# Performance work log

Measured on AMD Instinct MI355X. Metric: run time of the kernel, lower is better.

Reference implementation:

```python
import math
import jax, jax.numpy as jnp
import numpy as np

NUM_HEADS = 12


def _key_blocks(x, w):
    # x: [B,S,H,D] -> overlapping key blocks [B, C, 3w, H, D], block c covers
    # original key positions [c*w - w, c*w + 2w) (zero padded at the edges).
    B, S, H, D = x.shape
    C = S // w
    x_pad = jnp.pad(x, ((0, 0), (w, w), (0, 0), (0, 0)))
    idx = (jnp.arange(C) * w)[:, None] + jnp.arange(3 * w)[None, :]  # [C,3w]
    return x_pad[:, idx]


def _band_qk(q, k, w):
    # banded_gemm_qk: scores[b,i,h,j] = q[b,i,h,:] . k[b,i+j-w,h,:], j in [0,2w]
    B, S, H, D = q.shape
    C = S // w
    kb = _key_blocks(k, w)                       # [B,C,3w,H,D]
    qb = q.reshape(B, C, w, H, D)
    s = jnp.einsum('bcxhd,bcyhd->bchxy', qb, kb)  # [B,C,H,w,3w]
    row = jnp.arange(w)[:, None]
    col = row + jnp.arange(2 * w + 1)[None, :]    # diagonal extraction
    band = s[:, :, :, row, col]                   # [B,C,H,w,2w+1]
    return band.transpose(0, 1, 3, 2, 4).reshape(B, S, H, 2 * w + 1)


def _band_pv(p, v, w):
    # banded_gemm_pv: out[b,i,h,:] = sum_j p[b,i,h,j] * v[b,i+j-w,h,:]
    B, S, H, M = p.shape
    C = S // w
    vb = _key_blocks(v, w)                        # [B,C,3w,H,D]
    pb = p.reshape(B, C, w, H, M).transpose(0, 1, 3, 2, 4)  # [B,C,H,w,2w+1]
    row = jnp.arange(w)[:, None]
    col = row + jnp.arange(2 * w + 1)[None, :]
    p_full = jnp.zeros((B, C, H, w, 3 * w), p.dtype).at[:, :, :, row, col].set(pb)
    out = jnp.einsum('bchxy,bcyhd->bcxhd', p_full, vb)  # [B,C,w,H,D]
    return out.reshape(B, S, H, -1)


def setup_inputs():
    key = jax.random.key(0)
    ks = jax.random.split(key, 14)
    B, S, E, G = 2, 4096, 768, 64
    scale = 0.02
    hs = jax.random.normal(ks[0], (B, S, E), jnp.float32)
    mask = jnp.zeros((B, 1, 1, S), jnp.int32).at[:, :, :, :G].set(1)
    def lin(k):
        kw, kb = jax.random.split(k)
        return (jax.random.normal(kw, (E, E), jnp.float32) * scale,
                jax.random.normal(kb, (E,), jnp.float32) * scale)
    Wq, bq = lin(ks[1]); Wk, bk = lin(ks[2]); Wv, bv = lin(ks[3])
    Wqg, bqg = lin(ks[4]); Wkg, bkg = lin(ks[5]); Wvg, bvg = lin(ks[6])
    return dict(hidden_states=hs, attention_mask=mask,
                Wq=Wq, bq=bq, Wk=Wk, bk=bk, Wv=Wv, bv=bv,
                Wqg=Wqg, bqg=bqg, Wkg=Wkg, bkg=bkg, Wvg=Wvg, bvg=bvg,
                window=256, num_global=G)


def reference(hidden_states, attention_mask, Wq, bq, Wk, bk, Wv, bv,
              Wqg, bqg, Wkg, bkg, Wvg, bvg, window, num_global):
    B, S, E = hidden_states.shape
    H = NUM_HEADS
    D = E // H
    w, G = window, num_global
    inv_sqrt_d = 1.0 / math.sqrt(D)

    mask2d = attention_mask.reshape(B, S)
    removed = mask2d != 0  # global (or padding) keys excluded from windowed attn

    q = (hidden_states @ Wq + bq) * inv_sqrt_d
    k = hidden_states @ Wk + bk
    v = hidden_states @ Wv + bv
    q = q.reshape(B, S, H, D)
    k = k.reshape(B, S, H, D)
    v = v.reshape(B, S, H, D)

    # --- local (banded) attention scores ---
    band = _band_qk(q, k, w)                                  # [B,S,H,2w+1]
    key_pos = jnp.arange(S)[:, None] + jnp.arange(-w, w + 1)[None, :]  # [S,2w+1]
    valid = (key_pos >= 0) & (key_pos < S)
    removed_pad = jnp.pad(removed, ((0, 0), (w, w)))
    band_removed = removed_pad[:, key_pos + w]                # [B,S,2w+1]
    keep = valid[None, :, None, :] & (~band_removed)[:, :, None, :]
    band = jnp.where(keep, band, -jnp.inf)

    # --- every-token -> global-token scores (global tokens are first G) ---
    sel = jnp.einsum('blhd,bshd->blhs', q, k[:, :G])          # [B,S,H,G]
    scores = jnp.concatenate([sel, band], axis=-1)            # [B,S,H,G+2w+1]
    probs = jax.nn.softmax(scores.astype(jnp.float32), axis=-1)

    out = jnp.einsum('blhs,bshd->blhd', probs[..., :G], v[:, :G].astype(jnp.float32))
    out = out + _band_pv(probs[..., G:], v.astype(jnp.float32), w)
    out = out.astype(hidden_states.dtype).reshape(B, S, E)

    # --- global tokens attend to everything (separate projections) ---
    hg = hidden_states[:, :G]
    qg = (hg @ Wqg + bqg).reshape(B, G, H, D)
    kg = (hidden_states @ Wkg + bkg).reshape(B, S, H, D)
    vg = (hidden_states @ Wvg + bvg).reshape(B, S, H, D)
    gs = jnp.einsum('bghd,bshd->bhgs', qg, kg) * inv_sqrt_d   # [B,H,G,S]
    gp = jax.nn.softmax(gs.astype(jnp.float32), axis=-1)
    go = jnp.einsum('bhgs,bshd->bghd', gp, vg.astype(jnp.float32)).reshape(B, G, E)
    out = out.at[:, :G].set(go.astype(out.dtype))
    return out
```

## Files before the change

### kernel.cpp

```cpp
#include <hip/hip_runtime.h>
#include <hip/hip_bf16.h>


#define BB 2
#define SS 4096
#define EE 768
#define HH 12
#define DD 64
#define WW 256
#define GG 64
#define NSPLIT 16

typedef unsigned short u16;
typedef __attribute__((ext_vector_type(4))) float f4v;
typedef __attribute__((ext_vector_type(8))) short s8v;
typedef __attribute__((ext_vector_type(4))) int i4v;
typedef __attribute__((ext_vector_type(4))) unsigned short us4v;

#define MFMA_BF16(a, b, c) __builtin_amdgcn_mfma_f32_16x16x32_bf16((a), (b), (c), 0, 0, 0)

constexpr long NSE     = (long)BB * SS * EE;
constexpr long OFF_HSB = 0;
constexpr long OFF_WT  = OFF_HSB + NSE;
constexpr long OFF_Q   = OFF_WT + 6L * EE * EE;
constexpr long OFF_K   = OFF_Q + NSE;
constexpr long OFF_V   = OFF_K + NSE;
constexpr long OFF_KG  = OFF_V + NSE;
constexpr long OFF_VG  = OFF_KG + NSE;
constexpr long OFF_QG  = OFF_VG + NSE;
constexpr long OFF_VT  = OFF_QG + (long)BB * GG * EE;
constexpr long OFF_VGT = OFF_VT + NSE;

constexpr long NQTILE = (long)BB * HH * 4;

__device__ __forceinline__ u16 f2bf(float f) {
  unsigned u = __float_as_uint(f);
  u += 0x7fffu + ((u >> 16) & 1u);
  return (u16)(u >> 16);
}

__global__ __launch_bounds__(256) void k_prep(const float* __restrict__ hs,
                                              const float* __restrict__ Wq, const float* __restrict__ Wk,
                                              const float* __restrict__ Wv, const float* __restrict__ Wkg,
                                              const float* __restrict__ Wvg, const float* __restrict__ Wqg,
                                              u16* __restrict__ ws) {
  int bid = blockIdx.x;
  if (bid < 6144) {
    long i = ((long)bid * 256 + threadIdx.x) * 4;
    f4v v = *(const f4v*)(hs + i);
    us4v o;
#pragma unroll
    for (int j = 0; j < 4; ++j) o[j] = f2bf(v[j]);
    *(us4v*)(ws + OFF_HSB + i) = o;
    return;
  }
  int wb = bid - 6144;
  int widx = wb / 576; int rem = wb % 576; int kt = rem / 24; int nt = rem % 24;
  const float* src;
  switch (widx) {
    case 0: src = Wq; break; case 1: src = Wk; break; case 2: src = Wv; break;
    case 3: src = Wkg; break; case 4: src = Wvg; break; default: src = Wqg; break;
  }
  __shared__ float tl[32][33];
  int t = threadIdx.x; int r = t >> 3; int c4 = (t & 7) * 4;
  f4v v = *(const f4v*)(src + (long)(kt * 32 + r) * EE + nt * 32 + c4);
#pragma unroll
  for (int j = 0; j < 4; ++j) tl[r][c4 + j] = v[j];
  __syncthreads();
  us4v o;
#pragma unroll
  for (int j = 0; j < 4; ++j) o[j] = f2bf(tl[c4 + j][r]);
  *(us4v*)(ws + OFF_WT + (long)widx * EE * EE + (long)(nt * 32 + r) * EE + kt * 32 + c4) = o;
}

__global__ __launch_bounds__(256, 4) void k_proj(u16* __restrict__ ws,
                                              const float* __restrict__ bq, const float* __restrict__ bk,
                                              const float* __restrict__ bv, const float* __restrict__ bkg,
                                              const float* __restrict__ bvg, const float* __restrict__ bqg) {
  int bid = blockIdx.x;
  int widx, mt, nt;
  if (bid < 1920) {
    int L = (bid & 7) * 240 + (bid >> 3);
    mt = L / 30; int inner = L % 30; widx = inner / 6; nt = inner % 6;
  } else { widx = 5; mt = 0; nt = bid - 1920; }

  __shared__ u16 Al[128 * 64];
  __shared__ u16 Bl[128 * 64];
  int tid = threadIdx.x, lane = tid & 63, wid = tid >> 6;
  int wr = wid >> 1, wc = wid & 1;

  f4v acc[4][4];
#pragma unroll
  for (int i = 0; i < 4; ++i)
#pragma unroll
    for (int j = 0; j < 4; ++j) acc[i][j] = f4v{0.f, 0.f, 0.f, 0.f};

  const u16* hsb = ws + OFF_HSB;
  const u16* Wp  = ws + OFF_WT + (long)widx * EE * EE;

  const u16* asrc[4]; const u16* bsrc[4];
  int dso[4];
#pragma unroll
  for (int it = 0; it < 4; ++it) {
    int c = tid + it * 256;
    int r = c >> 3, j = c & 7;
    long arow;
    if (widx == 5) { int rr = mt * 128 + r; arow = (long)(rr >> 6) * SS + (rr & 63); }
    else           { arow = (long)mt * 128 + r; }
    asrc[it] = hsb + arow * EE + j * 8;
    bsrc[it] = Wp + (long)(nt * 128 + r) * EE + j * 8;
    dso[it]  = r * 64 + (j ^ (r & 7)) * 8;
  }

  const u16* afp[4]; const u16* bfp[4];
#pragma unroll
  for (int f = 0; f < 4; ++f) {
    afp[f] = Al + (wr * 64 + f * 16 + (lane & 15)) * 64;
    bfp[f] = Bl + (wc * 64 + f * 16 + (lane & 15)) * 64;
  }
  int hi4 = lane >> 4, lx = lane & 7;

  i4v areg[4], breg[4];
#pragma unroll
  for (int it = 0; it < 4; ++it) {
    areg[it] = *(const i4v*)(asrc[it]);
    breg[it] = *(const i4v*)(bsrc[it]);
  }
#pragma unroll
  for (int it = 0; it < 4; ++it) {
    *(i4v*)&Al[dso[it]] = areg[it];
    *(i4v*)&Bl[dso[it]] = breg[it];
  }
  __syncthreads();

  for (int t = 0; t < 12; ++t) {
    if (t < 11) {
      int k0n = (t + 1) * 64;
#pragma unroll
      for (int it = 0; it < 4; ++it) {
        areg[it] = *(const i4v*)(asrc[it] + k0n);
        breg[it] = *(const i4v*)(bsrc[it] + k0n);
      }
    }
#pragma unroll
    for (int ks = 0; ks < 2; ++ks) {
      int sw = ((ks * 4 + hi4) ^ lx) * 8;
      s8v af[4], bfr[4];
#pragma unroll
      for (int f = 0; f < 4; ++f) {
        af[f]  = *(const s8v*)(afp[f] + sw);
        bfr[f] = *(const s8v*)(bfp[f] + sw);
      }
#pragma unroll
      for (int i = 0; i < 4; ++i)
#pragma unroll
        for (int j = 0; j < 4; ++j) acc[i][j] = MFMA_BF16(af[i], bfr[j], acc[i][j]);
    }
    __syncthreads();
    if (t < 11) {
#pragma unroll
      for (int it = 0; it < 4; ++it) {
        *(i4v*)&Al[dso[it]] = areg[it];
        *(i4v*)&Bl[dso[it]] = breg[it];
      }
    }
    __syncthreads();
  }

  const float* bias; u16* outp; float scl = 1.0f;
  switch (widx) {
    case 0: bias = bq;  outp = ws + OFF_Q;  scl = 0.125f * 1.44269504f; break;
    case 1: bias = bk;  outp = ws + OFF_K;  break;
    case 2: bias = bv;  outp = ws + OFF_VT;  break;
    case 3: bias = bkg; outp = ws + OFF_KG; break;
    case 4: bias = bvg; outp = ws + OFF_VGT; break;
    default: bias = bqg; outp = ws + OFF_QG; scl = 0.125f; break;
  }

  if (widx == 2 || widx == 4) {
    int s0g = mt * 128 + wr * 64 + (lane >> 4) * 4;
#pragma unroll
    for (int fi = 0; fi < 4; ++fi) {
      int srow = s0g + fi * 16;
      int b_ = srow >> 12; int sl = srow & (SS - 1);
#pragma unroll
      for (int fj = 0; fj < 4; ++fj) {
        int col = nt * 128 + wc * 64 + fj * 16 + (lane & 15);
        float bcol = bias[col];
        us4v o;
#pragma unroll
        for (int e = 0; e < 4; ++e) o[e] = f2bf(acc[fi][fj][e] + bcol);
        *(us4v*)&outp[((long)(b_ * HH + (col >> 6)) * DD + (col & 63)) * SS + sl] = o;
      }
    }
  } else {
#pragma unroll
    for (int fi = 0; fi < 4; ++fi)
#pragma unroll
      for (int fj = 0; fj < 4; ++fj) {
        int col = nt * 128 + wc * 64 + fj * 16 + (lane & 15);
        float bcol = bias[col];
#pragma unroll
        for (int e = 0; e < 4; ++e) {
          int rl = wr * 64 + fi * 16 + (lane >> 4) * 4 + e;
          float vv = (acc[fi][fj][e] + bcol) * scl;
          outp[(long)(mt * 128 + rl) * EE + col] = f2bf(vv);
        }
      }
  }
}

__global__ __launch_bounds__(256) void k_lattn(const u16* __restrict__ ws, float* __restrict__ out) {
  int bid0 = blockIdx.x;
  int bid = (bid0 & 7) * 189 + (bid0 >> 3);
  int b = bid / (HH * 63); int rem = bid % (HH * 63); int h = rem / 63; int qt = rem % 63;
  int l0 = GG + qt * 64;
  int tid = threadIdx.x, lane = tid & 63, wid = tid >> 6;

  __shared__ u16 Kl[64][72];
  __shared__ u16 Vtl[64][72];
  __shared__ u16 Pl[4][16][72];

  const u16* Qp  = ws + OFF_Q + (long)b * SS * EE;
  const u16* Kp  = ws + OFF_K + (long)b * SS * EE;
  const u16* Vtp = ws + OFF_VT + (long)(b * HH + h) * DD * SS;

  int qbase = l0 + wid * 16;
  s8v qf[2];
#pragma unroll
  for (int ks = 0; ks < 2; ++ks)
    qf[ks] = *(const s8v*)(Qp + (long)(qbase + (lane & 15)) * EE + h * DD + ks * 32 + (lane >> 4) * 8);

  float m_r[4], l_p[4]; f4v ao[4];
#pragma unroll
  for (int e = 0; e < 4; ++e) { m_r[e] = -1e30f; l_p[e] = 0.f; }
#pragma unroll
  for (int df = 0; df < 4; ++df) ao[df] = f4v{0.f, 0.f, 0.f, 0.f};

  int lo = (l0 - WW > GG) ? (l0 - WW) : GG;
  int hi = (l0 + 64 + WW < SS) ? (l0 + 64 + WW) : SS;
  int ntile = 1 + ((hi - lo) >> 6);

  const u16* kbase[2]; const u16* vbase[2];
  u16* kdst[2]; u16* vdst[2];
#pragma unroll
  for (int it = 0; it < 2; ++it) {
    int c = tid + it * 256;
    int sr = c >> 3, so = (c & 7) * 8;
    kbase[it] = Kp + (long)sr * EE + h * DD + so;
    vbase[it] = Vtp + (long)sr * SS + so;
    kdst[it] = &Kl[sr][so];
    vdst[it] = &Vtl[sr][so];
  }

  i4v kreg[2], vreg[2];
#pragma unroll
  for (int it = 0; it < 2; ++it) {
    kreg[it] = *(const i4v*)(kbase[it]);
    vreg[it] = *(const i4v*)(vbase[it]);
  }
#pragma unroll
  for (int it = 0; it < 2; ++it) {
    *(i4v*)kdst[it] = kreg[it];
    *(i4v*)vdst[it] = vreg[it];
  }
  __syncthreads();

  for (int t = 0; t < ntile; ++t) {
    int kb = (t == 0) ? 0 : lo + (t - 1) * 64;
    if (t + 1 < ntile) {
      int kbn = lo + t * 64;
#pragma unroll
      for (int it = 0; it < 2; ++it) {
        kreg[it] = *(const i4v*)(kbase[it] + (long)kbn * EE);
        vreg[it] = *(const i4v*)(vbase[it] + kbn);
      }
    }

    f4v sc[4];
#pragma unroll
    for (int c = 0; c < 4; ++c) sc[c] = f4v{0.f, 0.f, 0.f, 0.f};
    __builtin_amdgcn_s_setprio(1);
#pragma unroll
    for (int c = 0; c < 4; ++c)
#pragma unroll
      for (int ks = 0; ks < 2; ++ks) {
        s8v kf = *(const s8v*)&Kl[c * 16 + (lane & 15)][ks * 32 + (lane >> 4) * 8];
        sc[c] = MFMA_BF16(qf[ks], kf, sc[c]);
      }
    __builtin_amdgcn_s_setprio(0);

    if (t > 0 && (kb <= l0 - WW || kb >= l0 + WW)) {
#pragma unroll
      for (int c = 0; c < 4; ++c) {
        int key = kb + c * 16 + (lane & 15);
#pragma unroll
        for (int e = 0; e < 4; ++e) {
          int qrow = qbase + (lane >> 4) * 4 + e;
          if (key < qrow - WW || key > qrow + WW) sc[c][e] = -1e30f;
        }
      }
    }

    float pmax[4];
#pragma unroll
    for (int e = 0; e < 4; ++e)
      pmax[e] = fmaxf(fmaxf(sc[0][e], sc[1][e]), fmaxf(sc[2][e], sc[3][e]));
    bool need;
    if (t == 0) need = true;
    else {
      bool ok = (pmax[0] <= m_r[0] + 11.5f) & (pmax[1] <= m_r[1] + 11.5f) &
                (pmax[2] <= m_r[2] + 11.5f) & (pmax[3] <= m_r[3] + 11.5f);
      need = !__all(ok);
    }
    if (need) {
#pragma unroll
      for (int e = 0; e < 4; ++e) {
        float rm = pmax[e];
#pragma unroll
        for (int off = 1; off < 16; off <<= 1) rm = fmaxf(rm, __shfl_xor(rm, off));
        float mn = fmaxf(m_r[e], rm);
        float scl = exp2f(m_r[e] - mn);
        l_p[e] *= scl;
#pragma unroll
        for (int df = 0; df < 4; ++df) ao[df][e] *= scl;
        m_r[e] = mn;
      }
    }

#pragma unroll
    for (int e = 0; e < 4; ++e) {
      float p0 = exp2f(sc[0][e] - m_r[e]);
      float p1 = exp2f(sc[1][e] - m_r[e]);
      float p2 = exp2f(sc[2][e] - m_r[e]);
      float p3 = exp2f(sc[3][e] - m_r[e]);
      l_p[e] += (p0 + p1) + (p2 + p3);
      int pr = (lane >> 4) * 4 + e;
      Pl[wid][pr][(lane & 15)]      = f2bf(p0);
      Pl[wid][pr][16 + (lane & 15)] = f2bf(p1);
      Pl[wid][pr][32 + (lane & 15)] = f2bf(p2);
      Pl[wid][pr][48 + (lane & 15)] = f2bf(p3);
    }

    __builtin_amdgcn_s_setprio(1);
#pragma unroll
    for (int kblk = 0; kblk < 2; ++kblk) {
      s8v pf = *(const s8v*)&Pl[wid][lane & 15][kblk * 32 + (lane >> 4) * 8];
#pragma unroll
      for (int df = 0; df < 4; ++df) {
        s8v vf = *(const s8v*)&Vtl[df * 16 + (lane & 15)][kblk * 32 + (lane >> 4) * 8];
        ao[df] = MFMA_BF16(pf, vf, ao[df]);
      }
    }
    __builtin_amdgcn_s_setprio(0);
    __syncthreads();

    if (t + 1 < ntile) {
#pragma unroll
      for (int it = 0; it < 2; ++it) {
        *(i4v*)kdst[it] = kreg[it];
        *(i4v*)vdst[it] = vreg[it];
      }
    }
    __syncthreads();
  }

  float l_r[4];
#pragma unroll
  for (int e = 0; e < 4; ++e) {
    float s = l_p[e];
#pragma unroll
    for (int off = 1; off < 16; off <<= 1) s += __shfl_xor(s, off);
    l_r[e] = s;
  }
#pragma unroll
  for (int df = 0; df < 4; ++df)
#pragma unroll
    for (int e = 0; e < 4; ++e) {
      int row = qbase + (lane >> 4) * 4 + e;
      int col = h * DD + df * 16 + (lane & 15);
      out[((long)b * SS + row) * EE + col] = ao[df][e] / l_r[e];
    }
}

__global__ __launch_bounds__(64) void k_gattn_part(u16* __restrict__ ws) {
  int bid = blockIdx.x;
  int g = bid / NSPLIT; int sp = bid % NSPLIT;
  int b = g / (HH * 4); int rem = g % (HH * 4); int h = rem >> 2; int qs = rem & 3;
  int lane = threadIdx.x;

  __shared__ u16 Kl[32][72];
  __shared__ u16 Vtl[64][40];
  __shared__ u16 Pl[16][40];

  const u16* Qgp = ws + OFF_QG + (long)b * GG * EE;
  const u16* Kgp = ws + OFF_KG + (long)b * SS * EE;
  const u16* Vtp = ws + OFF_VGT + (long)(b * HH + h) * DD * SS;

  int qbase = qs * 16;
  s8v qf[2];
#pragma unroll
  for (int ks = 0; ks < 2; ++ks)
    qf[ks] = *(const s8v*)(Qgp + (long)(qbase + (lane & 15)) * EE + h * DD + ks * 32 + (lane >> 4) * 8);

  float m_r[4], l_r[4]; f4v ao[4];
#pragma unroll
  for (int e = 0; e < 4; ++e) { m_r[e] = -1e30f; l_r[e] = 0.f; }
#pragma unroll
  for (int df = 0; df < 4; ++df) ao[df] = f4v{0.f, 0.f, 0.f, 0.f};

  int t0 = sp * (SS / 32 / NSPLIT);
  for (int kt = t0; kt < t0 + SS / 32 / NSPLIT; ++kt) {
    int kb = kt * 32;
#pragma unroll
    for (int r2 = 0; r2 < 4; ++r2) {
      int chunk = lane + r2 * 64;
      int kr = chunk >> 3, ko = (chunk & 7) * 8;
      *(i4v*)&Kl[kr][ko] = *(const i4v*)(Kgp + (long)(kb + kr) * EE + h * DD + ko);
      int dr = chunk >> 2, ko2 = (chunk & 3) * 8;
      *(i4v*)&Vtl[dr][ko2] = *(const i4v*)(Vtp + (long)dr * SS + kb + ko2);
    }
    __syncthreads();

    f4v sc[2] = {f4v{0.f, 0.f, 0.f, 0.f}, f4v{0.f, 0.f, 0.f, 0.f}};
#pragma unroll
    for (int c = 0; c < 2; ++c)
#pragma unroll
      for (int ks = 0; ks < 2; ++ks) {
        s8v kf = *(const s8v*)&Kl[c * 16 + (lane & 15)][ks * 32 + (lane >> 4) * 8];
        sc[c] = MFMA_BF16(qf[ks], kf, sc[c]);
      }

    float scl_[4], p0[4], p1[4];
#pragma unroll
    for (int e = 0; e < 4; ++e) {
      float rm = fmaxf(sc[0][e], sc[1][e]);
#pragma unroll
      for (int off = 1; off < 16; off <<= 1) rm = fmaxf(rm, __shfl_xor(rm, off));
      float mn = fmaxf(m_r[e], rm);
      scl_[e] = __expf(m_r[e] - mn);
      p0[e] = __expf(sc[0][e] - mn);
      p1[e] = __expf(sc[1][e] - mn);
      float s = p0[e] + p1[e];
#pragma unroll
      for (int off = 1; off < 16; off <<= 1) s += __shfl_xor(s, off);
      l_r[e] = l_r[e] * scl_[e] + s;
      m_r[e] = mn;
    }
#pragma unroll
    for (int df = 0; df < 4; ++df)
#pragma unroll
      for (int e = 0; e < 4; ++e) ao[df][e] *= scl_[e];

#pragma unroll
    for (int e = 0; e < 4; ++e) {
      Pl[(lane >> 4) * 4 + e][lane & 15]        = f2bf(p0[e]);
      Pl[(lane >> 4) * 4 + e][16 + (lane & 15)] = f2bf(p1[e]);
    }
    s8v pf = *(const s8v*)&Pl[lane & 15][(lane >> 4) * 8];
#pragma unroll
    for (int df = 0; df < 4; ++df) {
      s8v vf = *(const s8v*)&Vtl[df * 16 + (lane & 15)][(lane >> 4) * 8];
      ao[df] = MFMA_BF16(pf, vf, ao[df]);
    }
    __syncthreads();
  }

  float* PA = (float*)(ws + OFF_V);
  float* Pm = PA + NQTILE * NSPLIT * 1024L;
  float* Pl2 = Pm + NQTILE * NSPLIT * 16L;
  long pb = (long)g * NSPLIT + sp;
#pragma unroll
  for (int df = 0; df < 4; ++df)
#pragma unroll
    for (int e = 0; e < 4; ++e) {
      int rl = (lane >> 4) * 4 + e;
      PA[pb * 1024 + rl * 64 + df * 16 + (lane & 15)] = ao[df][e];
    }
  if ((lane & 15) == 0) {
#pragma unroll
    for (int e = 0; e < 4; ++e) {
      int rl = (lane >> 4) * 4 + e;
      Pm[pb * 16 + rl] = m_r[e];
      Pl2[pb * 16 + rl] = l_r[e];
    }
  }
}

__global__ __launch_bounds__(256) void k_gattn_comb(const u16* __restrict__ ws, float* __restrict__ out) {
  int g = blockIdx.x;
  int b = g / (HH * 4); int rem = g % (HH * 4); int h = rem >> 2; int qs = rem & 3;
  int tid = threadIdx.x;
  int row = tid >> 4; int c4 = (tid & 15) * 4;

  const float* PA = (const float*)(ws + OFF_V);
  const float* Pm = PA + NQTILE * NSPLIT * 1024L;
  const float* Pl2 = Pm + NQTILE * NSPLIT * 16L;
  long base = (long)g * NSPLIT;

  float M = -1e30f;
#pragma unroll
  for (int s = 0; s < NSPLIT; ++s) M = fmaxf(M, Pm[(base + s) * 16 + row]);
  f4v acc = f4v{0.f, 0.f, 0.f, 0.f};
  float L = 0.f;
#pragma unroll
  for (int s = 0; s < NSPLIT; ++s) {
    float wgt = __expf(Pm[(base + s) * 16 + row] - M);
    L += wgt * Pl2[(base + s) * 16 + row];
    f4v a = *(const f4v*)&PA[(base + s) * 1024 + row * 64 + c4];
#pragma unroll
    for (int j = 0; j < 4; ++j) acc[j] += wgt * a[j];
  }
  float inv = 1.f / L;
  f4v o;
#pragma unroll
  for (int j = 0; j < 4; ++j) o[j] = acc[j] * inv;
  *(f4v*)&out[((long)b * SS + qs * 16 + row) * EE + h * DD + c4] = o;
}

extern "C" void kernel_launch(void* const* d_in, const int* in_sizes, int n_in,
                              void* d_out, int out_size, void* d_ws, size_t ws_size,
                              hipStream_t stream) {
  const float* hs  = (const float*)d_in[0];
  const float* Wq  = (const float*)d_in[2];  const float* bq  = (const float*)d_in[3];
  const float* Wk  = (const float*)d_in[4];  const float* bk  = (const float*)d_in[5];
  const float* Wv  = (const float*)d_in[6];  const float* bv  = (const float*)d_in[7];
  const float* Wqg = (const float*)d_in[8];  const float* bqg = (const float*)d_in[9];
  const float* Wkg = (const float*)d_in[10]; const float* bkg = (const float*)d_in[11];
  const float* Wvg = (const float*)d_in[12]; const float* bvg = (const float*)d_in[13];
  u16* ws = (u16*)d_ws;
  float* out = (float*)d_out;

  k_prep<<<6144 + 6 * 24 * 24, 256, 0, stream>>>(hs, Wq, Wk, Wv, Wkg, Wvg, Wqg, ws);
  k_proj<<<1926, 256, 0, stream>>>(ws, bq, bk, bv, bkg, bvg, bqg);
  k_gattn_part<<<(int)(NQTILE * NSPLIT), 64, 0, stream>>>(ws);
  k_gattn_comb<<<(int)NQTILE, 256, 0, stream>>>(ws, out);
  k_lattn<<<BB * HH * 63, 256, 0, stream>>>(ws, out);
}
```

Baseline: 154.8 us.

## Fold global-attention combine into local-attention launch and add lazy rescaling

The separate combine kernel for global-query partial results is merged into k_lattn as extra tail blocks, removing one kernel launch. The global partial kernel switches to base-2 exponentials, with the scale folded into Qg. It also skips the online-softmax rescale when the tile max stays within a threshold of the running max, and defers the row-sum shuffle reduction to the end. Probabilities are packed to bf16 in pairs with a hardware conversion intrinsic. The lazy rescale lets values grow up to about 2^11.5 before renormalising, which trades a little precision headroom for fewer shuffles and exponentials.

```diff
diff --git a/kernel.cpp b/kernel.cpp
--- a/kernel.cpp
+++ b/kernel.cpp
@@ -32,11 +32,18 @@
 constexpr long OFF_VGT = OFF_VT + NSE;
 
 constexpr long NQTILE = (long)BB * HH * 4;
+constexpr int  NLB    = BB * HH * 63;
 
 __device__ __forceinline__ u16 f2bf(float f) {
   unsigned u = __float_as_uint(f);
   u += 0x7fffu + ((u >> 16) & 1u);
   return (u16)(u >> 16);
+}
+
+__device__ __forceinline__ unsigned pk_bf16(float a, float b) {
+  union { __hip_bfloat162 h; unsigned u; } c;
+  c.h = __float22bfloat162_rn(make_float2(a, b));
+  return c.u;
 }
 
 __global__ __launch_bounds__(256) void k_prep(const float* __restrict__ hs,
@@ -174,7 +181,7 @@
     case 2: bias = bv;  outp = ws + OFF_VT;  break;
     case 3: bias = bkg; outp = ws + OFF_KG; break;
     case 4: bias = bvg; outp = ws + OFF_VGT; break;
-    default: bias = bqg; outp = ws + OFF_QG; scl = 0.125f; break;
+    default: bias = bqg; outp = ws + OFF_QG; scl = 0.125f * 1.44269504f; break;
   }
 
   if (widx == 2 || widx == 4) {
@@ -212,6 +219,38 @@
 
 __global__ __launch_bounds__(256) void k_lattn(const u16* __restrict__ ws, float* __restrict__ out) {
   int bid0 = blockIdx.x;
+  if (bid0 >= NLB) {
+    int g = bid0 - NLB;
+    int b = g / (HH * 4); int rem = g % (HH * 4); int h = rem >> 2; int qs = rem & 3;
+    int tid = threadIdx.x;
+    int row = tid >> 4; int c4 = (tid & 15) * 4;
+
+    const float* PA = (const float*)(ws + OFF_V);
+    const float* Pm = PA + NQTILE * NSPLIT * 1024L;
+    const float* Pl2 = Pm + NQTILE * NSPLIT * 16L;
+    long base = (long)g * NSPLIT;
+
+    float M = -1e30f;
+#pragma unroll
+    for (int s = 0; s < NSPLIT; ++s) M = fmaxf(M, Pm[(base + s) * 16 + row]);
+    f4v acc = f4v{0.f, 0.f, 0.f, 0.f};
+    float L = 0.f;
+#pragma unroll
+    for (int s = 0; s < NSPLIT; ++s) {
+      float wgt = exp2f(Pm[(base + s) * 16 + row] - M);
+      L += wgt * Pl2[(base + s) * 16 + row];
+      f4v a = *(const f4v*)&PA[(base + s) * 1024 + row * 64 + c4];
+#pragma unroll
+      for (int j = 0; j < 4; ++j) acc[j] += wgt * a[j];
+    }
+    float inv = 1.f / L;
+    f4v o;
+#pragma unroll
+    for (int j = 0; j < 4; ++j) o[j] = acc[j] * inv;
+    *(f4v*)&out[((long)b * SS + qs * 16 + row) * EE + h * DD + c4] = o;
+    return;
+  }
+
   int bid = (bid0 & 7) * 189 + (bid0 >> 3);
   int b = bid / (HH * 63); int rem = bid % (HH * 63); int h = rem / 63; int qt = rem % 63;
   int l0 = GG + qt * 64;
@@ -335,11 +374,14 @@
       float p2 = exp2f(sc[2][e] - m_r[e]);
       float p3 = exp2f(sc[3][e] - m_r[e]);
       l_p[e] += (p0 + p1) + (p2 + p3);
+      unsigned u01 = pk_bf16(p0, p1);
+      unsigned u23 = pk_bf16(p2, p3);
       int pr = (lane >> 4) * 4 + e;
-      Pl[wid][pr][(lane & 15)]      = f2bf(p0);
-      Pl[wid][pr][16 + (lane & 15)] = f2bf(p1);
-      Pl[wid][pr][32 + (lane & 15)] = f2bf(p2);
-      Pl[wid][pr][48 + (lane & 15)] = f2bf(p3);
+      int l15 = lane & 15;
+      Pl[wid][pr][l15]      = (u16)u01;
+      Pl[wid][pr][16 + l15] = (u16)(u01 >> 16);
+      Pl[wid][pr][32 + l15] = (u16)u23;
+      Pl[wid][pr][48 + l15] = (u16)(u23 >> 16);
     }
 
     __builtin_amdgcn_s_setprio(1);
@@ -403,9 +445,9 @@
   for (int ks = 0; ks < 2; ++ks)
     qf[ks] = *(const s8v*)(Qgp + (long)(qbase + (lane & 15)) * EE + h * DD + ks * 32 + (lane >> 4) * 8);
 
-  float m_r[4], l_r[4]; f4v ao[4];
-#pragma unroll
-  for (int e = 0; e < 4; ++e) { m_r[e] = -1e30f; l_r[e] = 0.f; }
+  float m_r[4], l_p[4]; f4v ao[4];
+#pragma unroll
+  for (int e = 0; e < 4; ++e) { m_r[e] = -1e30f; l_p[e] = 0.f; }
 #pragma unroll
   for (int df = 0; df < 4; ++df) ao[df] = f4v{0.f, 0.f, 0.f, 0.f};
 
@@ -431,31 +473,41 @@
         sc[c] = MFMA_BF16(qf[ks], kf, sc[c]);
       }
 
-    float scl_[4], p0[4], p1[4];
+    float pmax[4];
+#pragma unroll
+    for (int e = 0; e < 4; ++e) pmax[e] = fmaxf(sc[0][e], sc[1][e]);
+    bool need;
+    if (kt == t0) need = true;
+    else {
+      bool ok = (pmax[0] <= m_r[0] + 11.5f) & (pmax[1] <= m_r[1] + 11.5f) &
+                (pmax[2] <= m_r[2] + 11.5f) & (pmax[3] <= m_r[3] + 11.5f);
+      need = !__all(ok);
+    }
+    if (need) {
+#pragma unroll
+      for (int e = 0; e < 4; ++e) {
+        float rm = pmax[e];
+#pragma unroll
+        for (int off = 1; off < 16; off <<= 1) rm = fmaxf(rm, __shfl_xor(rm, off));
+        float mn = fmaxf(m_r[e], rm);
+        float scl = exp2f(m_r[e] - mn);
+        l_p[e] *= scl;
+#pragma unroll
+        for (int df = 0; df < 4; ++df) ao[df][e] *= scl;
+        m_r[e] = mn;
+      }
+    }
+
 #pragma unroll
     for (int e = 0; e < 4; ++e) {
-      float rm = fmaxf(sc[0][e], sc[1][e]);
-#pragma unroll
-      for (int off = 1; off < 16; off <<= 1) rm = fmaxf(rm, __shfl_xor(rm, off));
-      float mn = fmaxf(m_r[e], rm);
-      scl_[e] = __expf(m_r[e] - mn);
-      p0[e] = __expf(sc[0][e] - mn);
-      p1[e] = __expf(sc[1][e] - mn);
-      float s = p0[e] + p1[e];
-#pragma unroll
-      for (int off = 1; off < 16; off <<= 1) s += __shfl_xor(s, off);
-      l_r[e] = l_r[e] * scl_[e] + s;
-      m_r[e] = mn;
-    }
-#pragma unroll
-    for (int df = 0; df < 4; ++df)
-#pragma unroll
-      for (int e = 0; e < 4; ++e) ao[df][e] *= scl_[e];
-
-#pragma unroll
-    for (int e = 0; e < 4; ++e) {
-      Pl[(lane >> 4) * 4 + e][lane & 15]        = f2bf(p0[e]);
-      Pl[(lane >> 4) * 4 + e][16 + (lane & 15)] = f2bf(p1[e]);
+      float p0 = exp2f(sc[0][e] - m_r[e]);
+      float p1 = exp2f(sc[1][e] - m_r[e]);
+      l_p[e] += p0 + p1;
+      unsigned u01 = pk_bf16(p0, p1);
+      int pr = (lane >> 4) * 4 + e;
+      int l15 = lane & 15;
+      Pl[pr][l15]      = (u16)u01;
+      Pl[pr][16 + l15] = (u16)(u01 >> 16);
     }
     s8v pf = *(const s8v*)&Pl[lane & 15][(lane >> 4) * 8];
 #pragma unroll
@@ -464,6 +516,15 @@
       ao[df] = MFMA_BF16(pf, vf, ao[df]);
     }
     __syncthreads();
+  }
+
+  float l_r[4];
+#pragma unroll
+  for (int e = 0; e < 4; ++e) {
+    float s = l_p[e];
+#pragma unroll
+    for (int off = 1; off < 16; off <<= 1) s += __shfl_xor(s, off);
+    l_r[e] = s;
   }
 
   float* PA = (float*)(ws + OFF_V);
@@ -485,37 +546,6 @@
       Pl2[pb * 16 + rl] = l_r[e];
     }
   }
-}
-
-__global__ __launch_bounds__(256) void k_gattn_comb(const u16* __restrict__ ws, float* __restrict__ out) {
-  int g = blockIdx.x;
-  int b = g / (HH * 4); int rem = g % (HH * 4); int h = rem >> 2; int qs = rem & 3;
-  int tid = threadIdx.x;
-  int row = tid >> 4; int c4 = (tid & 15) * 4;
-
-  const float* PA = (const float*)(ws + OFF_V);
-  const float* Pm = PA + NQTILE * NSPLIT * 1024L;
-  const float* Pl2 = Pm + NQTILE * NSPLIT * 16L;
-  long base = (long)g * NSPLIT;
-
-  float M = -1e30f;
-#pragma unroll
-  for (int s = 0; s < NSPLIT; ++s) M = fmaxf(M, Pm[(base + s) * 16 + row]);
-  f4v acc = f4v{0.f, 0.f, 0.f, 0.f};
-  float L = 0.f;
-#pragma unroll
-  for (int s = 0; s < NSPLIT; ++s) {
-    float wgt = __expf(Pm[(base + s) * 16 + row] - M);
-    L += wgt * Pl2[(base + s) * 16 + row];
-    f4v a = *(const f4v*)&PA[(base + s) * 1024 + row * 64 + c4];
-#pragma unroll
-    for (int j = 0; j < 4; ++j) acc[j] += wgt * a[j];
-  }
-  float inv = 1.f / L;
-  f4v o;
-#pragma unroll
-  for (int j = 0; j < 4; ++j) o[j] = acc[j] * inv;
-  *(f4v*)&out[((long)b * SS + qs * 16 + row) * EE + h * DD + c4] = o;
 }
 
 extern "C" void kernel_launch(void* const* d_in, const int* in_sizes, int n_in,
@@ -534,6 +564,5 @@
   k_prep<<<6144 + 6 * 24 * 24, 256, 0, stream>>>(hs, Wq, Wk, Wv, Wkg, Wvg, Wqg, ws);
   k_proj<<<1926, 256, 0, stream>>>(ws, bq, bk, bv, bkg, bvg, bqg);
   k_gattn_part<<<(int)(NQTILE * NSPLIT), 64, 0, stream>>>(ws);
-  k_gattn_comb<<<(int)NQTILE, 256, 0, stream>>>(ws, out);
-  k_lattn<<<BB * HH * 63, 256, 0, stream>>>(ws, out);
-}
+  k_lattn<<<NLB + (int)NQTILE, 256, 0, stream>>>(ws, out);
+}
```

Result: faster. 136.0 us (-12.2%).
